# Optimization experiments

Hardware: AMD Instinct MI355X
Metric: run time of the kernel (lower is better)

The kernel has to match this reference:

```python
import jax, jax.numpy as jnp
import numpy as np

R_S, R_T = 16, 8
D_SEG, D_GLB = 64, 128
H_SEG, H_GLB = 2, 4
NL = 2
FF_SEG, FF_GLB = 128, 256
THRESH = 0.5
B, L = 16, 1024


def setup_inputs() -> dict:
    key = jax.random.key(0)
    ks = iter(jax.random.split(key, 40))

    def p(shape, s=0.02):
        return s * jax.random.normal(next(ks), shape, dtype=jnp.float32)

    inp = {}
    inp['pts'] = jax.random.normal(next(ks), (B, L, 3), dtype=jnp.float32)
    # Fourier spatio-temporal encoder params
    inp['fs'] = p((2, R_S), 1.0)                      # spatial frequencies
    inp['ft'] = p((R_T,), 1.0)                        # temporal frequencies
    inp['w_space'] = p((2 * R_S, D_SEG)); inp['b_space'] = p((D_SEG,))
    inp['w_time'] = p((2 * R_T, 32)); inp['b_time'] = p((32,))
    inp['w_fout'] = p((D_SEG + 32, D_SEG)); inp['b_fout'] = p((D_SEG,))
    # gating
    inp['w_gate'] = p((D_SEG,), 1.0); inp['b_gate'] = p(())
    # segment mini-transformer (2 post-norm encoder layers, relu FFN)
    inp['seg_attn_w'] = p((NL, 4, D_SEG, D_SEG)); inp['seg_attn_b'] = p((NL, 4, D_SEG))
    inp['seg_ln_g'] = jnp.ones((NL, 2, D_SEG), jnp.float32)
    inp['seg_ln_b'] = jnp.zeros((NL, 2, D_SEG), jnp.float32)
    inp['seg_ff1_w'] = p((NL, D_SEG, FF_SEG)); inp['seg_ff1_b'] = p((NL, FF_SEG))
    inp['seg_ff2_w'] = p((NL, FF_SEG, D_SEG)); inp['seg_ff2_b'] = p((NL, D_SEG))
    # global aggregator transformer
    inp['glb_attn_w'] = p((NL, 4, D_GLB, D_GLB)); inp['glb_attn_b'] = p((NL, 4, D_GLB))
    inp['glb_ln_g'] = jnp.ones((NL, 2, D_GLB), jnp.float32)
    inp['glb_ln_b'] = jnp.zeros((NL, 2, D_GLB), jnp.float32)
    inp['glb_ff1_w'] = p((NL, D_GLB, FF_GLB)); inp['glb_ff1_b'] = p((NL, FF_GLB))
    inp['glb_ff2_w'] = p((NL, FF_GLB, D_GLB)); inp['glb_ff2_b'] = p((NL, D_GLB))
    # projections
    inp['up_w'] = p((D_SEG, D_GLB)); inp['up_b'] = p((D_GLB,))
    inp['fin_w'] = p((D_GLB, D_GLB)); inp['fin_b'] = p((D_GLB,))
    return inp


def _ln(x, g, b, eps=1e-5):
    m = x.mean(-1, keepdims=True)
    v = ((x - m) ** 2).mean(-1, keepdims=True)
    return (x - m) * jax.lax.rsqrt(v + eps) * g + b


def _mha(x, mask, w, bb, nh):
    Bb, S, D = x.shape
    hd = D // nh
    wq, wk, wv, wo = w
    bq, bk, bv, bo = bb
    q = (x @ wq + bq).reshape(Bb, S, nh, hd)
    k = (x @ wk + bk).reshape(Bb, S, nh, hd)
    v = (x @ wv + bv).reshape(Bb, S, nh, hd)
    sc = jnp.einsum('bqhd,bkhd->bhqk', q, k) / jnp.sqrt(jnp.float32(hd))
    sc = jnp.where(mask[:, None, :, :], sc, jnp.float32(-1e9))
    a = jax.nn.softmax(sc, axis=-1)
    o = jnp.einsum('bhqk,bkhd->bqhd', a, v).reshape(Bb, S, D)
    return o @ wo + bo


def _encoder(x, mask, attn_w, attn_b, ln_g, ln_b, ff1_w, ff1_b, ff2_w, ff2_b, nh):
    # PyTorch-style post-norm TransformerEncoder (dropout=0, eval mode)
    for l in range(attn_w.shape[0]):
        x = _ln(x + _mha(x, mask, attn_w[l], attn_b[l], nh), ln_g[l, 0], ln_b[l, 0])
        h = jax.nn.relu(x @ ff1_w[l] + ff1_b[l]) @ ff2_w[l] + ff2_b[l]
        x = _ln(x + h, ln_g[l, 1], ln_b[l, 1])
    return x


def reference(pts, fs, ft, w_space, b_space, w_time, b_time, w_fout, b_fout, w_gate, b_gate, seg_attn_w, seg_attn_b, seg_ln_g, seg_ln_b, seg_ff1_w, seg_ff1_b, seg_ff2_w, seg_ff2_b, glb_attn_w, glb_attn_b, glb_ln_g, glb_ln_b, glb_ff1_w, glb_ff1_b, glb_ff2_w, glb_ff2_b, up_w, up_b, fin_w, fin_b):
    Bb, Ll, _ = pts.shape
    two_pi = jnp.float32(2.0 * np.pi)
    xy, t = pts[..., :2], pts[..., 2:3]
    # Fourier features (space + time), fused into d=64 point embedding z
    sp = xy @ fs * two_pi                                        # [B,L,r_s]
    sp_feat = jnp.concatenate([jnp.sin(sp), jnp.cos(sp)], -1) @ w_space + b_space
    tp = t * ft * two_pi                                         # [B,L,r_t]
    t_feat = jnp.concatenate([jnp.sin(tp), jnp.cos(tp)], -1) @ w_time + b_time
    z = jnp.concatenate([sp_feat, t_feat], -1) @ w_fout + b_fout  # [B,L,64]

    # dynamic segmentation gating: boundary where sigmoid gate > threshold
    gate = jax.nn.sigmoid(z @ w_gate + b_gate)                   # [B,L]
    boundary = (gate > THRESH).at[:, 0].set(True)
    seg_id = jnp.cumsum(boundary.astype(jnp.int32), axis=1) - 1  # [B,L] contiguous ids
    n_seg = seg_id[:, -1] + 1                                    # [B]

    # segment mini-transformer == full-length transformer with within-segment attention mask
    seg_mask = seg_id[:, :, None] == seg_id[:, None, :]          # [B,L,L]
    h = _encoder(z, seg_mask, seg_attn_w, seg_attn_b, seg_ln_g, seg_ln_b,
                 seg_ff1_w, seg_ff1_b, seg_ff2_w, seg_ff2_b, H_SEG)

    # per-segment mean pooling (padded to L segment slots)
    sums = jax.vmap(lambda hh, sid: jax.ops.segment_sum(hh, sid, num_segments=Ll))(h, seg_id)
    cnts = jax.vmap(lambda sid: jax.ops.segment_sum(jnp.ones((Ll,), jnp.float32), sid, num_segments=Ll))(seg_id)
    seg_emb = sums / jnp.maximum(cnts, 1.0)[..., None]           # [B,L,64]
    valid = jnp.arange(Ll)[None, :] < n_seg[:, None]             # [B,L]
    seg_emb = jnp.where(valid[..., None], seg_emb @ up_w + up_b, 0.0)  # [B,L,128]

    # global aggregator over valid segment embeddings (padding-masked)
    glb_mask = (valid[:, None, :] & valid[:, :, None]) | jnp.eye(Ll, dtype=bool)[None]
    g = _encoder(seg_emb, glb_mask, glb_attn_w, glb_attn_b, glb_ln_g, glb_ln_b,
                 glb_ff1_w, glb_ff1_b, glb_ff2_w, glb_ff2_b, H_GLB)
    agg = (g * valid[..., None]).sum(1) / n_seg[:, None].astype(jnp.float32)

    # single-segment trajectories skip the global aggregator
    global_emb = jnp.where((n_seg == 1)[:, None], seg_emb[:, 0, :], agg)
    return global_emb @ fin_w + fin_b                            # [B,128]
```

## Files before the change

### kernel.cpp

```cpp
#include <hip/hip_runtime.h>
#include <math.h>

#define B_ 16
#define L_ 1024
#define M_TOT (B_*L_)

typedef __attribute__((ext_vector_type(8))) short short8v;
typedef __attribute__((ext_vector_type(4))) float f32x4;

__device__ __forceinline__ float wave_reduce_sum(float v) {
#pragma unroll
  for (int o = 32; o >= 1; o >>= 1) v += __shfl_xor(v, o, 64);
  return v;
}

__device__ __forceinline__ unsigned short f2bf(float f) {
  union { float f; unsigned u; } v; v.f = f;
  unsigned r = v.u + 0x7FFFu + ((v.u >> 16) & 1u);
  return (unsigned short)(r >> 16);
}

__global__ __launch_bounds__(256) void pack_all_kernel(
    const float* __restrict__ s0, const float* __restrict__ s1,
    const float* __restrict__ s2, const float* __restrict__ s3,
    const float* __restrict__ s4, const float* __restrict__ s5,
    const float* __restrict__ s6, unsigned short* __restrict__ wpk)
{
  int idx = blockIdx.x*256 + (int)threadIdx.x;
  const float* src; unsigned short* dst; int K, N;
  if      (idx <  4096) { src=s0; dst=wpk;          K=64;  N=64;  }
  else if (idx <  6144) { src=s1; dst=wpk+32768;    K=64;  N=128; idx-=4096; }
  else if (idx <  8192) { src=s2; dst=wpk+49152;    K=128; N=64;  idx-=6144; }
  else if (idx < 24576) { src=s3; dst=wpk+65536;    K=128; N=128; idx-=8192; }
  else if (idx < 32768) { src=s4; dst=wpk+196608;   K=128; N=256; idx-=24576; }
  else if (idx < 40960) { src=s5; dst=wpk+262144;   K=256; N=128; idx-=32768; }
  else if (idx < 41984) { src=s6; dst=wpk+327680;   K=64;  N=128; idx-=40960; }
  else return;
  const int l = idx & 63;
  int f = idx >> 6;
  const int ntn = N >> 4;
  const int nt = f % ntn; f /= ntn;
  const int ktn = K >> 5;
  const int kt = f % ktn;
  const int m  = f / ktn;
  const float* s = src + (size_t)m*K*N + (size_t)(kt*32 + ((l>>4)<<3))*N + nt*16 + (l&15);
  unsigned pw[4];
#pragma unroll
  for (int jj = 0; jj < 4; ++jj)
    pw[jj] = (unsigned)f2bf(s[(size_t)(2*jj)*N]) | ((unsigned)f2bf(s[(size_t)(2*jj+1)*N]) << 16);
  uint4 u; u.x = pw[0]; u.y = pw[1]; u.z = pw[2]; u.w = pw[3];
  *reinterpret_cast<uint4*>(dst + (size_t)idx*8) = u;
}

template<int K, int PN, int NPARTS, bool RELU, bool GATED, bool WF32, bool WBF, int SPART = -1>
__global__ __launch_bounds__(256) void mgemm_kernel(
    const unsigned short* __restrict__ Abf,
    const unsigned short* __restrict__ Wpk,
    const float* __restrict__ bias,
    float* __restrict__ C, unsigned short* __restrict__ Cbf,
    const int* __restrict__ nseg)
{
  constexpr int NOUT = NPARTS*PN;
  constexpr int KT = K/32;
  constexpr int NTP = PN/16;
  constexpr int CPP = PN/64;
  const int row0 = blockIdx.x * 64;
  if (GATED) { const int b = row0 >> 10; if ((row0 & (L_-1)) >= nseg[b]) return; }
  const int ct = blockIdx.y;
  const int part = ct / CPP;
  const int nt0  = (ct % CPP) * 4;
  const int wv = (int)threadIdx.x >> 6;
  const int ln = (int)threadIdx.x & 63;
  const int rbase = row0 + wv*16;
  const unsigned short* aptr = Abf + (size_t)(rbase + (ln & 15))*K + ((ln >> 4) << 3);
  const unsigned short* bptr = Wpk + ((size_t)part*KT*NTP + nt0)*512 + (size_t)ln*8;
  f32x4 acc0 = {0.f,0.f,0.f,0.f}, acc1 = {0.f,0.f,0.f,0.f};
  f32x4 acc2 = {0.f,0.f,0.f,0.f}, acc3 = {0.f,0.f,0.f,0.f};
#pragma unroll
  for (int kt = 0; kt < KT; ++kt) {
    short8v a = *reinterpret_cast<const short8v*>(aptr + kt*32);
    const unsigned short* bk = bptr + (size_t)kt*NTP*512;
    short8v b0 = *reinterpret_cast<const short8v*>(bk);
    short8v b1 = *reinterpret_cast<const short8v*>(bk + 512);
    short8v b2 = *reinterpret_cast<const short8v*>(bk + 1024);
    short8v b3 = *reinterpret_cast<const short8v*>(bk + 1536);
    acc0 = __builtin_amdgcn_mfma_f32_16x16x32_bf16(a, b0, acc0, 0, 0, 0);
    acc1 = __builtin_amdgcn_mfma_f32_16x16x32_bf16(a, b1, acc1, 0, 0, 0);
    acc2 = __builtin_amdgcn_mfma_f32_16x16x32_bf16(a, b2, acc2, 0, 0, 0);
    acc3 = __builtin_amdgcn_mfma_f32_16x16x32_bf16(a, b3, acc3, 0, 0, 0);
  }
  const int colb = part*PN + nt0*16 + (ln & 15);
  const int rowe = rbase + ((ln >> 4) << 2);
  f32x4 av[4] = {acc0, acc1, acc2, acc3};
#pragma unroll
  for (int i = 0; i < 4; ++i) {
    const int col = colb + i*16;
    const float bs = bias[col];
#pragma unroll
    for (int r = 0; r < 4; ++r) {
      float v = av[i][r] + bs;
      if (SPART >= 0) { if (part == SPART) v *= 0.25506972533f; }
      if (RELU) v = fmaxf(v, 0.f);
      if (WF32) C[(size_t)(rowe + r)*NOUT + col] = v;
      if (WBF)  Cbf[(size_t)(rowe + r)*NOUT + col] = f2bf(v);
    }
  }
}

template<int K>
__global__ __launch_bounds__(256) void mgemm_ln64_kernel(
    const unsigned short* __restrict__ Abf,
    const unsigned short* __restrict__ Wpk,
    const float* __restrict__ bias,
    float* __restrict__ x,
    const float* __restrict__ gam, const float* __restrict__ bet,
    unsigned short* __restrict__ xbf)
{
  constexpr int KT = K/32;
  const int row0 = blockIdx.x * 64;
  const int wv = (int)threadIdx.x >> 6;
  const int ln = (int)threadIdx.x & 63;
  const int rbase = row0 + wv*16;
  const unsigned short* aptr = Abf + (size_t)(rbase + (ln & 15))*K + ((ln >> 4) << 3);
  const unsigned short* bptr = Wpk + (size_t)ln*8;
  f32x4 acc0 = {0.f,0.f,0.f,0.f}, acc1 = {0.f,0.f,0.f,0.f};
  f32x4 acc2 = {0.f,0.f,0.f,0.f}, acc3 = {0.f,0.f,0.f,0.f};
#pragma unroll
  for (int kt = 0; kt < KT; ++kt) {
    short8v a = *reinterpret_cast<const short8v*>(aptr + kt*32);
    const unsigned short* bk = bptr + (size_t)kt*4*512;
    short8v b0 = *reinterpret_cast<const short8v*>(bk);
    short8v b1 = *reinterpret_cast<const short8v*>(bk + 512);
    short8v b2 = *reinterpret_cast<const short8v*>(bk + 1024);
    short8v b3 = *reinterpret_cast<const short8v*>(bk + 1536);
    acc0 = __builtin_amdgcn_mfma_f32_16x16x32_bf16(a, b0, acc0, 0, 0, 0);
    acc1 = __builtin_amdgcn_mfma_f32_16x16x32_bf16(a, b1, acc1, 0, 0, 0);
    acc2 = __builtin_amdgcn_mfma_f32_16x16x32_bf16(a, b2, acc2, 0, 0, 0);
    acc3 = __builtin_amdgcn_mfma_f32_16x16x32_bf16(a, b3, acc3, 0, 0, 0);
  }
  const int colc = ln & 15;
  const int rowe = rbase + ((ln >> 4) << 2);
  f32x4 av[4] = {acc0, acc1, acc2, acc3};
  float v[4][4];
#pragma unroll
  for (int i = 0; i < 4; ++i) {
    const int col = i*16 + colc;
    const float bs = bias[col];
#pragma unroll
    for (int r = 0; r < 4; ++r)
      v[i][r] = av[i][r] + bs + x[(size_t)(rowe + r)*64 + col];
  }
  float rs[4];
#pragma unroll
  for (int r = 0; r < 4; ++r) rs[r] = v[0][r]+v[1][r]+v[2][r]+v[3][r];
#pragma unroll
  for (int m = 1; m <= 8; m <<= 1)
#pragma unroll
    for (int r = 0; r < 4; ++r) rs[r] += __shfl_xor(rs[r], m, 64);
  float mean[4], vs[4];
#pragma unroll
  for (int r = 0; r < 4; ++r) { mean[r] = rs[r]*(1.0f/64.0f); vs[r] = 0.f; }
#pragma unroll
  for (int i = 0; i < 4; ++i)
#pragma unroll
    for (int r = 0; r < 4; ++r) { const float d = v[i][r]-mean[r]; vs[r] = fmaf(d, d, vs[r]); }
#pragma unroll
  for (int m = 1; m <= 8; m <<= 1)
#pragma unroll
    for (int r = 0; r < 4; ++r) vs[r] += __shfl_xor(vs[r], m, 64);
  float rstd[4];
#pragma unroll
  for (int r = 0; r < 4; ++r) rstd[r] = rsqrtf(vs[r]*(1.0f/64.0f) + 1e-5f);
#pragma unroll
  for (int i = 0; i < 4; ++i) {
    const int col = i*16 + colc;
    const float g = gam[col], bb = bet[col];
#pragma unroll
    for (int r = 0; r < 4; ++r) {
      const float out = (v[i][r]-mean[r])*rstd[r]*g + bb;
      x[(size_t)(rowe + r)*64 + col] = out;
      xbf[(size_t)(rowe + r)*64 + col] = f2bf(out);
    }
  }
}

__global__ __launch_bounds__(256) void featurize_kernel(
    const float* __restrict__ pts, const float* __restrict__ fs, const float* __restrict__ ft,
    const float* __restrict__ w_space, const float* __restrict__ b_space,
    const float* __restrict__ w_time, const float* __restrict__ b_time,
    const float* __restrict__ w_fout, const float* __restrict__ b_fout,
    const float* __restrict__ w_gate, const float* __restrict__ b_gate,
    float* __restrict__ z, unsigned short* __restrict__ zbf, int* __restrict__ boundary)
{
  const int sub = threadIdx.x >> 6;
  const int d   = threadIdx.x & 63;
  const int p   = blockIdx.x * 4 + sub;
  const float TWO_PI = 6.283185307179586f;
  __shared__ float feat[4][32];
  __shared__ float tfeat[4][16];
  __shared__ float g96[4][96];
  const float x = pts[p*3+0], y = pts[p*3+1], t = pts[p*3+2];
  if (d < 16) {
    float sp = (x*fs[d] + y*fs[16+d]) * TWO_PI;
    feat[sub][d]    = sinf(sp);
    feat[sub][16+d] = cosf(sp);
  } else if (d < 24) {
    int r = d - 16;
    float tp = t * ft[r] * TWO_PI;
    tfeat[sub][r]   = sinf(tp);
    tfeat[sub][8+r] = cosf(tp);
  }
  __syncthreads();
  float sf = b_space[d];
#pragma unroll
  for (int k2 = 0; k2 < 32; ++k2) sf = fmaf(feat[sub][k2], w_space[k2*64+d], sf);
  g96[sub][d] = sf;
  if (d < 32) {
    float tf = b_time[d];
#pragma unroll
    for (int k2 = 0; k2 < 16; ++k2) tf = fmaf(tfeat[sub][k2], w_time[k2*32+d], tf);
    g96[sub][64+d] = tf;
  }
  __syncthreads();
  float zv = b_fout[d];
#pragma unroll
  for (int k2 = 0; k2 < 96; ++k2) zv = fmaf(g96[sub][k2], w_fout[k2*64+d], zv);
  z[(size_t)p*64+d] = zv;
  zbf[(size_t)p*64+d] = f2bf(zv);
  float gv = wave_reduce_sum(zv * w_gate[d]);
  if (d == 0) {
    float logit = gv + b_gate[0];
    float gate = 1.0f / (1.0f + expf(-logit));
    int bnd = (gate > 0.5f) ? 1 : 0;
    if ((p & (L_-1)) == 0) bnd = 1;
    boundary[p] = bnd;
  }
}

__global__ __launch_bounds__(1024) void scan_kernel(const int* __restrict__ boundary,
    int* __restrict__ seg_id, int* __restrict__ seg_start, int* __restrict__ n_seg)
{
  __shared__ int sc[1024];
  const int b = blockIdx.x, l = threadIdx.x;
  const int v = boundary[b*L_ + l];
  sc[l] = v;
  __syncthreads();
  for (int off = 1; off < 1024; off <<= 1) {
    int add = (l >= off) ? sc[l - off] : 0;
    __syncthreads();
    sc[l] += add;
    __syncthreads();
  }
  const int sid = sc[l] - 1;
  seg_id[b*L_ + l] = sid;
  if (v) seg_start[b*(L_+1) + sid] = l;
  if (l == L_-1) {
    n_seg[b] = sid + 1;
    seg_start[b*(L_+1) + sid + 1] = L_;
  }
}

__global__ __launch_bounds__(256) void seg_attn_kernel(
    const float* __restrict__ qkv,
    const int* __restrict__ seg_id, const int* __restrict__ seg_start,
    unsigned short* __restrict__ aobf)
{
  const int gid = blockIdx.x * 256 + (int)threadIdx.x;
  const int sub = gid & 7;
  const int item = gid >> 3;
  const int h  = item & 1;
  const int pt = (item >> 1) & (L_-1);
  const int b  = item >> 11;
  const float scale = 0.17677669529663687f;
  float4 q4 = *reinterpret_cast<const float4*>(qkv + (size_t)(b*L_+pt)*192 + h*32 + sub*4);
  q4.x*=scale; q4.y*=scale; q4.z*=scale; q4.w*=scale;
  const int s  = seg_id[b*L_ + pt];
  const int j0 = seg_start[b*(L_+1) + s];
  const int j1 = seg_start[b*(L_+1) + s + 1];
  float lsum = 0.f;
  float4 acc = {0.f,0.f,0.f,0.f};
  for (int j = j0; j < j1; ++j) {
    const float* base = qkv + (size_t)(b*L_ + j)*192 + h*32 + sub*4;
    float4 k4 = *reinterpret_cast<const float4*>(base + 64);
    float4 v4 = *reinterpret_cast<const float4*>(base + 128);
    float dot = q4.x*k4.x;
    dot = fmaf(q4.y, k4.y, dot);
    dot = fmaf(q4.z, k4.z, dot);
    dot = fmaf(q4.w, k4.w, dot);
    dot += __shfl_xor(dot, 1, 64);
    dot += __shfl_xor(dot, 2, 64);
    dot += __shfl_xor(dot, 4, 64);
    const float p = __expf(fminf(dot, 30.f));
    lsum += p;
    acc.x = fmaf(p, v4.x, acc.x);
    acc.y = fmaf(p, v4.y, acc.y);
    acc.z = fmaf(p, v4.z, acc.z);
    acc.w = fmaf(p, v4.w, acc.w);
  }
  const float inv = 1.0f / lsum;
  unsigned* op = reinterpret_cast<unsigned*>(aobf + (size_t)(b*L_+pt)*64 + h*32 + sub*4);
  op[0] = (unsigned)f2bf(acc.x*inv) | ((unsigned)f2bf(acc.y*inv) << 16);
  op[1] = (unsigned)f2bf(acc.z*inv) | ((unsigned)f2bf(acc.w*inv) << 16);
}

__global__ __launch_bounds__(256) void kvpack_kernel(
    const unsigned short* __restrict__ qkvbf, const int* __restrict__ n_seg,
    unsigned short* __restrict__ vfrag, unsigned short* __restrict__ kfrag)
{
  int idx = blockIdx.x*256 + (int)threadIdx.x;
  const bool isK = idx >= (1 << 18);
  idx &= (1 << 18) - 1;
  const int lane = idx & 63;
  const int dt = (idx >> 6) & 1;
  const int c  = (idx >> 7) & 31;
  const int h  = (idx >> 12) & 3;
  const int b  = idx >> 14;
  if (c*32 >= n_seg[b]) return;
  if (isK) {
    const int key = c*32 + dt*16 + (lane & 15);
    const uint4 u = *reinterpret_cast<const uint4*>(
        qkvbf + (size_t)(b*L_ + key)*384 + 128 + h*32 + ((lane >> 4) << 3));
    *reinterpret_cast<uint4*>(kfrag + (size_t)idx*8) = u;
    return;
  }
  const int g = lane >> 4;
  const int dcol = lane & 15;
  unsigned short vals[8];
#pragma unroll
  for (int j = 0; j < 8; ++j) {
    const int key = c*32 + g*4 + (j & 3) + ((j >> 2) << 4);
    vals[j] = qkvbf[(size_t)(b*L_ + key)*384 + 256 + h*32 + dt*16 + dcol];
  }
  uint4 u;
  u.x = (unsigned)vals[0] | ((unsigned)vals[1] << 16);
  u.y = (unsigned)vals[2] | ((unsigned)vals[3] << 16);
  u.z = (unsigned)vals[4] | ((unsigned)vals[5] << 16);
  u.w = (unsigned)vals[6] | ((unsigned)vals[7] << 16);
  *reinterpret_cast<uint4*>(vfrag + (size_t)idx*8) = u;
}

__global__ __launch_bounds__(256) void glb_attn_mfma_kernel(
    const unsigned short* __restrict__ qkvbf,
    const unsigned short* __restrict__ kfrag,
    const unsigned short* __restrict__ vfrag,
    const int* __restrict__ n_seg,
    unsigned short* __restrict__ aobf)
{
  const int g64 = blockIdx.x & 63;
  const int qt  = blockIdx.x >> 6;
  const int h  = g64 & 3;
  const int b  = g64 >> 2;
  const int ns = n_seg[b];
  if (qt*64 >= ns) return;
  const int wv = (int)threadIdx.x >> 6;
  const int ln = (int)threadIdx.x & 63;
  const int g  = ln >> 4;
  const int qc = ln & 15;
  __shared__ float lsumS[4][16];

  const int q0 = qt*64 + wv*16;
  const short8v qf = *reinterpret_cast<const short8v*>(
      qkvbf + (size_t)(b*L_ + q0 + qc)*384 + h*32 + g*8);

  f32x4 O0 = {0.f,0.f,0.f,0.f}, O1 = {0.f,0.f,0.f,0.f};
  const f32x4 zz = {0.f,0.f,0.f,0.f};
  float lsum = 0.f;
  const unsigned short* kfb = kfrag + (size_t)((b*4 + h)*32)*1024 + (size_t)ln*8;
  const unsigned short* vfb = vfrag + (size_t)((b*4 + h)*32)*1024 + (size_t)ln*8;

  const int nfull = ns >> 5;
#pragma unroll 2
  for (int c = 0; c < nfull; ++c) {
    short8v kf0 = *reinterpret_cast<const short8v*>(kfb);
    short8v kf1 = *reinterpret_cast<const short8v*>(kfb + 512);
    short8v v0  = *reinterpret_cast<const short8v*>(vfb);
    short8v v1  = *reinterpret_cast<const short8v*>(vfb + 512);
    f32x4 s0 = __builtin_amdgcn_mfma_f32_16x16x32_bf16(kf0, qf, zz, 0, 0, 0);
    f32x4 s1 = __builtin_amdgcn_mfma_f32_16x16x32_bf16(kf1, qf, zz, 0, 0, 0);
    float p[8];
#pragma unroll
    for (int r = 0; r < 4; ++r) {
      const float e0 = exp2f(fminf(s0[r], 43.f));
      const float e1 = exp2f(fminf(s1[r], 43.f));
      p[r] = e0; p[4+r] = e1;
      lsum += e0 + e1;
    }
    short8v pf;
#pragma unroll
    for (int i = 0; i < 8; ++i) pf[i] = (short)f2bf(p[i]);
    O0 = __builtin_amdgcn_mfma_f32_16x16x32_bf16(pf, v0, O0, 0, 0, 0);
    O1 = __builtin_amdgcn_mfma_f32_16x16x32_bf16(pf, v1, O1, 0, 0, 0);
    kfb += 1024; vfb += 1024;
  }
  if (ns & 31) {
    short8v kf0 = *reinterpret_cast<const short8v*>(kfb);
    short8v kf1 = *reinterpret_cast<const short8v*>(kfb + 512);
    short8v v0  = *reinterpret_cast<const short8v*>(vfb);
    short8v v1  = *reinterpret_cast<const short8v*>(vfb + 512);
    f32x4 s0 = __builtin_amdgcn_mfma_f32_16x16x32_bf16(kf0, qf, zz, 0, 0, 0);
    f32x4 s1 = __builtin_amdgcn_mfma_f32_16x16x32_bf16(kf1, qf, zz, 0, 0, 0);
    const int k0 = nfull*32;
    float p[8];
#pragma unroll
    for (int r = 0; r < 4; ++r) {
      const int key0 = k0 + g*4 + r;
      const float e0 = (key0 < ns)      ? exp2f(fminf(s0[r], 43.f)) : 0.f;
      const float e1 = (key0 + 16 < ns) ? exp2f(fminf(s1[r], 43.f)) : 0.f;
      p[r] = e0; p[4+r] = e1;
      lsum += e0 + e1;
    }
    short8v pf;
#pragma unroll
    for (int i = 0; i < 8; ++i) pf[i] = (short)f2bf(p[i]);
    O0 = __builtin_amdgcn_mfma_f32_16x16x32_bf16(pf, v0, O0, 0, 0, 0);
    O1 = __builtin_amdgcn_mfma_f32_16x16x32_bf16(pf, v1, O1, 0, 0, 0);
  }
  lsum += __shfl_xor(lsum, 16, 64);
  lsum += __shfl_xor(lsum, 32, 64);
  if (ln < 16) lsumS[wv][ln] = lsum;
  __syncthreads();
  unsigned short* outp = aobf + (size_t)(b*L_ + q0 + g*4)*128 + h*32 + qc;
#pragma unroll
  for (int r = 0; r < 4; ++r) {
    const float inv = 1.0f / lsumS[wv][g*4 + r];
    outp[(size_t)r*128]      = f2bf(O0[r]*inv);
    outp[(size_t)r*128 + 16] = f2bf(O1[r]*inv);
  }
}

__global__ __launch_bounds__(256) void ln128_kernel(
    float* __restrict__ x, const float* __restrict__ r,
    const float* __restrict__ gam, const float* __restrict__ bet,
    const int* __restrict__ nseg, unsigned short* __restrict__ xbf)
{
  const int row0 = blockIdx.x*2;
  const int b = row0 >> 10;
  if ((row0 & (L_-1)) >= nseg[b]) return;
  const int sub = (int)threadIdx.x >> 7;
  const int d   = (int)threadIdx.x & 127;
  const int row = row0 + sub;
  const bool valid = (row & (L_-1)) < nseg[b];
  __shared__ float red[2][4];
  float val = 0.f;
  if (valid) val = x[(size_t)row*128 + d] + r[(size_t)row*128 + d];
  float s = wave_reduce_sum(val);
  if ((d & 63) == 0) red[sub][d >> 6] = s;
  __syncthreads();
  s = red[sub][0] + red[sub][1];
  const float mean = s * (1.0f/128.0f);
  const float dv = val - mean;
  float s2 = wave_reduce_sum(dv*dv);
  if ((d & 63) == 0) red[sub][2 + (d >> 6)] = s2;
  __syncthreads();
  s2 = red[sub][2] + red[sub][3];
  if (valid) {
    const float out = dv * rsqrtf(s2*(1.0f/128.0f) + 1e-5f) * gam[d] + bet[d];
    x[(size_t)row*128 + d] = out;
    xbf[(size_t)row*128 + d] = f2bf(out);
  }
}

__global__ __launch_bounds__(256) void pool_kernel(
    const float* __restrict__ h, const int* __restrict__ seg_start,
    const int* __restrict__ n_seg, unsigned short* __restrict__ meanbf)
{
  const int gs = blockIdx.x*4 + ((int)threadIdx.x >> 6);
  const int b = gs >> 10, s = gs & (L_-1);
  const int d = (int)threadIdx.x & 63;
  if (s >= n_seg[b]) return;
  const int j0 = seg_start[b*(L_+1)+s], j1 = seg_start[b*(L_+1)+s+1];
  float acc = 0.f;
  for (int j = j0; j < j1; ++j) acc += h[(size_t)(b*L_+j)*64 + d];
  meanbf[(size_t)gs*64 + d] = f2bf(acc / (float)(j1 - j0));
}

__global__ __launch_bounds__(128) void row0_kernel(
    const float* __restrict__ xg, float* __restrict__ semb0)
{
  semb0[blockIdx.x*128 + threadIdx.x] = xg[(size_t)blockIdx.x*L_*128 + threadIdx.x];
}

__global__ __launch_bounds__(128) void pool_final_kernel(
    const float* __restrict__ g, const int* __restrict__ n_seg,
    float* __restrict__ partial)
{
  const int b = blockIdx.x >> 4, c = blockIdx.x & 15;
  const int d = (int)threadIdx.x;
  const int ns = n_seg[b];
  const int i0 = c*64, i1 = min(ns, i0 + 64);
  float acc = 0.f;
  for (int i = i0; i < i1; ++i) acc += g[(size_t)(b*L_+i)*128 + d];
  partial[(size_t)blockIdx.x*128 + d] = acc;
}

__global__ __launch_bounds__(128) void final_kernel(
    const float* __restrict__ partial, const float* __restrict__ semb0,
    const int* __restrict__ n_seg, const float* __restrict__ fin_w,
    const float* __restrict__ fin_b, float* __restrict__ out)
{
  const int b = blockIdx.x, d = threadIdx.x;
  const int ns = n_seg[b];
  __shared__ float pl[128];
  float pooled;
  if (ns == 1) pooled = semb0[b*128 + d];
  else {
    float acc = 0.f;
#pragma unroll
    for (int c = 0; c < 16; ++c) acc += partial[(size_t)(b*16 + c)*128 + d];
    pooled = acc / (float)ns;
  }
  pl[d] = pooled;
  __syncthreads();
  float o = fin_b[d];
#pragma unroll 8
  for (int k2 = 0; k2 < 128; ++k2) o = fmaf(pl[k2], fin_w[k2*128+d], o);
  out[b*128+d] = o;
}

extern "C" void kernel_launch(void* const* d_in, const int* in_sizes, int n_in,
                              void* d_out, int out_size, void* d_ws, size_t ws_size,
                              hipStream_t stream) {
  const float* pts     = (const float*)d_in[0];
  const float* fs      = (const float*)d_in[1];
  const float* ft      = (const float*)d_in[2];
  const float* w_space = (const float*)d_in[3];
  const float* b_space = (const float*)d_in[4];
  const float* w_time  = (const float*)d_in[5];
  const float* b_time  = (const float*)d_in[6];
  const float* w_fout  = (const float*)d_in[7];
  const float* b_fout  = (const float*)d_in[8];
  const float* w_gate  = (const float*)d_in[9];
  const float* b_gate  = (const float*)d_in[10];
  const float* seg_attn_w = (const float*)d_in[11];
  const float* seg_attn_b = (const float*)d_in[12];
  const float* seg_ln_g   = (const float*)d_in[13];
  const float* seg_ln_b   = (const float*)d_in[14];
  const float* seg_ff1_w  = (const float*)d_in[15];
  const float* seg_ff1_b  = (const float*)d_in[16];
  const float* seg_ff2_w  = (const float*)d_in[17];
  const float* seg_ff2_b  = (const float*)d_in[18];
  const float* glb_attn_w = (const float*)d_in[19];
  const float* glb_attn_b = (const float*)d_in[20];
  const float* glb_ln_g   = (const float*)d_in[21];
  const float* glb_ln_b   = (const float*)d_in[22];
  const float* glb_ff1_w  = (const float*)d_in[23];
  const float* glb_ff1_b  = (const float*)d_in[24];
  const float* glb_ff2_w  = (const float*)d_in[25];
  const float* glb_ff2_b  = (const float*)d_in[26];
  const float* up_w    = (const float*)d_in[27];
  const float* up_b    = (const float*)d_in[28];
  const float* fin_w   = (const float*)d_in[29];
  const float* fin_b   = (const float*)d_in[30];

  char* ws = (char*)d_ws;
  float* zx   = (float*)(ws);
  unsigned short* xg_bf = (unsigned short*)(ws);
  float* qkv  = (float*)(ws + ((size_t)4  << 20));
  unsigned short* qkv_bf = (unsigned short*)(ws + ((size_t)4 << 20));
  float* tmp  = qkv;
  float* aob  = (float*)(ws + ((size_t)30 << 20));
  float* xg   = (float*)(ws + ((size_t)38 << 20));
  unsigned short* zx_bf = (unsigned short*)(ws + ((size_t)38 << 20));
  int* boundary  = (int*)(ws + ((size_t)46 << 20));
  int* seg_id    = boundary + M_TOT;
  int* seg_start = seg_id + M_TOT;
  int* n_seg     = seg_start + B_*(L_+1);
  float* semb0     = (float*)(ws + ((size_t)47 << 20));
  float* partial   = (float*)(ws + ((size_t)47 << 20) + 65536);
  unsigned short* tmp_bf = (unsigned short*)(ws + ((size_t)50 << 20));
  unsigned short* vfrag  = (unsigned short*)(ws + ((size_t)58 << 20));
  unsigned short* kfrag  = (unsigned short*)(ws + ((size_t)62 << 20));
  unsigned short* abf    = (unsigned short*)(ws + ((size_t)84 << 20));
  unsigned short* wpk    = (unsigned short*)(ws + ((size_t)88 << 20));

  unsigned short* wpk_segA  = wpk;
  unsigned short* wpk_segF1 = wpk + 32768;
  unsigned short* wpk_segF2 = wpk + 49152;
  unsigned short* wpk_glbA  = wpk + 65536;
  unsigned short* wpk_glbF1 = wpk + 196608;
  unsigned short* wpk_glbF2 = wpk + 262144;
  unsigned short* wpk_up    = wpk + 327680;

  pack_all_kernel<<<164, 256, 0, stream>>>(seg_attn_w, seg_ff1_w, seg_ff2_w,
                                           glb_attn_w, glb_ff1_w, glb_ff2_w, up_w, wpk);

  featurize_kernel<<<M_TOT/4, 256, 0, stream>>>(pts, fs, ft, w_space, b_space, w_time, b_time,
                                                w_fout, b_fout, w_gate, b_gate, zx, zx_bf, boundary);
  scan_kernel<<<B_, 1024, 0, stream>>>(boundary, seg_id, seg_start, n_seg);

  for (int l = 0; l < 2; ++l) {
    const float* ab = seg_attn_b + (size_t)l*4*64;
    mgemm_kernel<64,64,3,false,false,true,false><<<dim3(256,3),256,0,stream>>>(
        zx_bf, wpk_segA + (size_t)l*4*4096, ab, qkv, nullptr, nullptr);
    seg_attn_kernel<<<(M_TOT*2*8)/256, 256, 0, stream>>>(qkv, seg_id, seg_start, abf);
    mgemm_ln64_kernel<64><<<256,256,0,stream>>>(
        abf, wpk_segA + (size_t)(l*4+3)*4096, ab + 192,
        zx, seg_ln_g + l*128, seg_ln_b + l*128, zx_bf);
    mgemm_kernel<64,128,1,true,false,false,true><<<dim3(256,2),256,0,stream>>>(
        zx_bf, wpk_segF1 + (size_t)l*8192, seg_ff1_b + l*128, nullptr, tmp_bf, nullptr);
    mgemm_ln64_kernel<128><<<256,256,0,stream>>>(
        tmp_bf, wpk_segF2 + (size_t)l*8192, seg_ff2_b + l*64,
        zx, seg_ln_g + l*128 + 64, seg_ln_b + l*128 + 64, zx_bf);
  }

  pool_kernel<<<M_TOT/4, 256, 0, stream>>>(zx, seg_start, n_seg, abf);
  mgemm_kernel<64,128,1,false,true,true,true><<<dim3(256,2),256,0,stream>>>(
      abf, wpk_up, up_b, xg, xg_bf, n_seg);
  row0_kernel<<<B_, 128, 0, stream>>>(xg, semb0);

  for (int l = 0; l < 2; ++l) {
    const float* ab = glb_attn_b + (size_t)l*4*128;
    mgemm_kernel<128,128,3,false,true,false,true,0><<<dim3(256,6),256,0,stream>>>(
        xg_bf, wpk_glbA + (size_t)l*4*16384, ab, nullptr, qkv_bf, n_seg);
    kvpack_kernel<<<2048, 256, 0, stream>>>(qkv_bf, n_seg, vfrag, kfrag);
    glb_attn_mfma_kernel<<<B_*4*16, 256, 0, stream>>>(qkv_bf, kfrag, vfrag, n_seg, abf);
    mgemm_kernel<128,128,1,false,true,true,false><<<dim3(256,2),256,0,stream>>>(
        abf, wpk_glbA + (size_t)(l*4+3)*16384, ab + 384, tmp, nullptr, n_seg);
    ln128_kernel<<<M_TOT/2, 256, 0, stream>>>(xg, tmp, glb_ln_g + l*256, glb_ln_b + l*256, n_seg, xg_bf);
    mgemm_kernel<128,256,1,true,true,false,true><<<dim3(256,4),256,0,stream>>>(
        xg_bf, wpk_glbF1 + (size_t)l*32768, glb_ff1_b + l*256, nullptr, tmp_bf, n_seg);
    mgemm_kernel<256,128,1,false,true,true,false><<<dim3(256,2),256,0,stream>>>(
        tmp_bf, wpk_glbF2 + (size_t)l*32768, glb_ff2_b + l*128, aob, nullptr, n_seg);
    ln128_kernel<<<M_TOT/2, 256, 0, stream>>>(xg, aob, glb_ln_g + l*256 + 128, glb_ln_b + l*256 + 128, n_seg, xg_bf);
  }

  pool_final_kernel<<<B_*16, 128, 0, stream>>>(xg, n_seg, partial);
  final_kernel<<<B_, 128, 0, stream>>>(partial, semb0, n_seg, fin_w, fin_b, (float*)d_out);
}
```

Before: 284.5 us.

## Fuse QKV fragment packing, residual LayerNorm, and row0 copy into global GEMMs

The global QKV GEMM now writes Q as bf16 and scatters K and V straight into the MFMA fragment layouts, which removes the separate kvpack kernel and its round trip through a 384-wide qkv buffer. The output-projection and FF2 GEMMs become full-width 128-column kernels that add the residual and apply LayerNorm in registers, replacing the separate ln128 kernels and their fp32 temporaries. The up-projection GEMM also writes the segment-0 embedding, removing the row0 kernel. In exchange, the K/V scatter uses scattered 2-byte stores, and the fused LN GEMMs launch fewer blocks that each do more work.

```diff
diff --git a/kernel.cpp b/kernel.cpp
--- a/kernel.cpp
+++ b/kernel.cpp
@@ -52,13 +52,14 @@
   *reinterpret_cast<uint4*>(dst + (size_t)idx*8) = u;
 }
 
-template<int K, int PN, int NPARTS, bool RELU, bool GATED, bool WF32, bool WBF, int SPART = -1>
+template<int K, int PN, int NPARTS, bool RELU, bool GATED, bool WF32, bool WBF,
+         int SPART = -1, bool SEMB0 = false>
 __global__ __launch_bounds__(256) void mgemm_kernel(
     const unsigned short* __restrict__ Abf,
     const unsigned short* __restrict__ Wpk,
     const float* __restrict__ bias,
     float* __restrict__ C, unsigned short* __restrict__ Cbf,
-    const int* __restrict__ nseg)
+    const int* __restrict__ nseg, float* __restrict__ semb0)
 {
   constexpr int NOUT = NPARTS*PN;
   constexpr int KT = K/32;
@@ -101,8 +102,72 @@
       float v = av[i][r] + bs;
       if (SPART >= 0) { if (part == SPART) v *= 0.25506972533f; }
       if (RELU) v = fmaxf(v, 0.f);
-      if (WF32) C[(size_t)(rowe + r)*NOUT + col] = v;
-      if (WBF)  Cbf[(size_t)(rowe + r)*NOUT + col] = f2bf(v);
+      const int row = rowe + r;
+      if (WF32) C[(size_t)row*NOUT + col] = v;
+      if (WBF)  Cbf[(size_t)row*NOUT + col] = f2bf(v);
+      if (SEMB0) { if ((row & (L_-1)) == 0) semb0[(row >> 10)*NOUT + col] = v; }
+    }
+  }
+}
+
+__global__ __launch_bounds__(256) void mgemm_qkvfrag_kernel(
+    const unsigned short* __restrict__ Abf,
+    const unsigned short* __restrict__ Wpk,
+    const float* __restrict__ bias,
+    unsigned short* __restrict__ qbf,
+    unsigned short* __restrict__ kfrag,
+    unsigned short* __restrict__ vfrag,
+    const int* __restrict__ nseg)
+{
+  constexpr int K = 128, PN = 128, KT = 4, NTP = 8;
+  const int row0 = blockIdx.x * 64;
+  const int bb = row0 >> 10;
+  if ((row0 & (L_-1)) >= nseg[bb]) return;
+  const int ct = blockIdx.y;
+  const int part = ct >> 1;
+  const int nt0 = (ct & 1) * 4;
+  const int wv = (int)threadIdx.x >> 6;
+  const int ln = (int)threadIdx.x & 63;
+  const int qc = ln & 15;
+  const int rbase = row0 + wv*16;
+  const unsigned short* aptr = Abf + (size_t)(rbase + qc)*K + ((ln >> 4) << 3);
+  const unsigned short* bptr = Wpk + ((size_t)part*KT*NTP + nt0)*512 + (size_t)ln*8;
+  f32x4 acc[4];
+#pragma unroll
+  for (int i = 0; i < 4; ++i) acc[i] = f32x4{0.f,0.f,0.f,0.f};
+#pragma unroll
+  for (int kt = 0; kt < KT; ++kt) {
+    short8v a = *reinterpret_cast<const short8v*>(aptr + kt*32);
+    const unsigned short* bk = bptr + (size_t)kt*NTP*512;
+#pragma unroll
+    for (int i = 0; i < 4; ++i)
+      acc[i] = __builtin_amdgcn_mfma_f32_16x16x32_bf16(
+          a, *reinterpret_cast<const short8v*>(bk + i*512), acc[i], 0, 0, 0);
+  }
+  const int rowe = rbase + ((ln >> 4) << 2);
+#pragma unroll
+  for (int i = 0; i < 4; ++i) {
+    const int cl = (nt0 + i)*16 + qc;
+    const int h = cl >> 5, dh = cl & 31;
+    const float bs = bias[part*PN + cl];
+#pragma unroll
+    for (int r = 0; r < 4; ++r) {
+      float v = acc[i][r] + bs;
+      const int row = rowe + r;
+      const int key = row & (L_-1);
+      if (part == 0) {
+        v *= 0.25506972533f;
+        qbf[(size_t)row*128 + cl] = f2bf(v);
+      } else if (part == 1) {
+        const size_t idx = (((size_t)((bb*4 + h)*32 + (key>>5))*2 + ((key>>4)&1))*64
+                            + ((dh>>3)*16 + (key&15)))*8 + (dh&7);
+        kfrag[idx] = f2bf(v);
+      } else {
+        const int kk = key & 31;
+        const size_t idx = (((size_t)((bb*4 + h)*32 + (key>>5))*2 + (dh>>4))*64
+                            + (((kk&15)>>2)*16 + (dh&15)))*8 + ((kk>>4)*4 + (kk&3));
+        vfrag[idx] = f2bf(v);
+      }
     }
   }
 }
@@ -180,6 +245,81 @@
       const float out = (v[i][r]-mean[r])*rstd[r]*g + bb;
       x[(size_t)(rowe + r)*64 + col] = out;
       xbf[(size_t)(rowe + r)*64 + col] = f2bf(out);
+    }
+  }
+}
+
+template<int K>
+__global__ __launch_bounds__(256) void mgemm_ln128_kernel(
+    const unsigned short* __restrict__ Abf,
+    const unsigned short* __restrict__ Wpk,
+    const float* __restrict__ bias,
+    float* __restrict__ x,
+    const float* __restrict__ gam, const float* __restrict__ bet,
+    const int* __restrict__ nseg, unsigned short* __restrict__ xbf)
+{
+  constexpr int KT = K/32;
+  const int row0 = blockIdx.x * 64;
+  if ((row0 & (L_-1)) >= nseg[row0 >> 10]) return;
+  const int wv = (int)threadIdx.x >> 6;
+  const int ln = (int)threadIdx.x & 63;
+  const int qc = ln & 15;
+  const int rbase = row0 + wv*16;
+  const unsigned short* aptr = Abf + (size_t)(rbase + qc)*K + ((ln >> 4) << 3);
+  const unsigned short* bptr = Wpk + (size_t)ln*8;
+  f32x4 acc[8];
+#pragma unroll
+  for (int i = 0; i < 8; ++i) acc[i] = f32x4{0.f,0.f,0.f,0.f};
+#pragma unroll
+  for (int kt = 0; kt < KT; ++kt) {
+    short8v a = *reinterpret_cast<const short8v*>(aptr + kt*32);
+    const unsigned short* bk = bptr + (size_t)kt*8*512;
+#pragma unroll
+    for (int i = 0; i < 8; ++i)
+      acc[i] = __builtin_amdgcn_mfma_f32_16x16x32_bf16(
+          a, *reinterpret_cast<const short8v*>(bk + i*512), acc[i], 0, 0, 0);
+  }
+  const int rowe = rbase + ((ln >> 4) << 2);
+  float v[8][4];
+#pragma unroll
+  for (int i = 0; i < 8; ++i) {
+    const int col = i*16 + qc;
+    const float bs = bias[col];
+#pragma unroll
+    for (int r = 0; r < 4; ++r)
+      v[i][r] = acc[i][r] + bs + x[(size_t)(rowe + r)*128 + col];
+  }
+  float rs[4];
+#pragma unroll
+  for (int r = 0; r < 4; ++r)
+    rs[r] = ((v[0][r]+v[1][r])+(v[2][r]+v[3][r])) + ((v[4][r]+v[5][r])+(v[6][r]+v[7][r]));
+#pragma unroll
+  for (int m = 1; m <= 8; m <<= 1)
+#pragma unroll
+    for (int r = 0; r < 4; ++r) rs[r] += __shfl_xor(rs[r], m, 64);
+  float mean[4], vs[4];
+#pragma unroll
+  for (int r = 0; r < 4; ++r) { mean[r] = rs[r]*(1.0f/128.0f); vs[r] = 0.f; }
+#pragma unroll
+  for (int i = 0; i < 8; ++i)
+#pragma unroll
+    for (int r = 0; r < 4; ++r) { const float d = v[i][r]-mean[r]; vs[r] = fmaf(d, d, vs[r]); }
+#pragma unroll
+  for (int m = 1; m <= 8; m <<= 1)
+#pragma unroll
+    for (int r = 0; r < 4; ++r) vs[r] += __shfl_xor(vs[r], m, 64);
+  float rstd[4];
+#pragma unroll
+  for (int r = 0; r < 4; ++r) rstd[r] = rsqrtf(vs[r]*(1.0f/128.0f) + 1e-5f);
+#pragma unroll
+  for (int i = 0; i < 8; ++i) {
+    const int col = i*16 + qc;
+    const float g = gam[col], bb = bet[col];
+#pragma unroll
+    for (int r = 0; r < 4; ++r) {
+      const float out = (v[i][r]-mean[r])*rstd[r]*g + bb;
+      x[(size_t)(rowe + r)*128 + col] = out;
+      xbf[(size_t)(rowe + r)*128 + col] = f2bf(out);
     }
   }
 }
@@ -303,44 +443,8 @@
   op[1] = (unsigned)f2bf(acc.z*inv) | ((unsigned)f2bf(acc.w*inv) << 16);
 }
 
-__global__ __launch_bounds__(256) void kvpack_kernel(
-    const unsigned short* __restrict__ qkvbf, const int* __restrict__ n_seg,
-    unsigned short* __restrict__ vfrag, unsigned short* __restrict__ kfrag)
-{
-  int idx = blockIdx.x*256 + (int)threadIdx.x;
-  const bool isK = idx >= (1 << 18);
-  idx &= (1 << 18) - 1;
-  const int lane = idx & 63;
-  const int dt = (idx >> 6) & 1;
-  const int c  = (idx >> 7) & 31;
-  const int h  = (idx >> 12) & 3;
-  const int b  = idx >> 14;
-  if (c*32 >= n_seg[b]) return;
-  if (isK) {
-    const int key = c*32 + dt*16 + (lane & 15);
-    const uint4 u = *reinterpret_cast<const uint4*>(
-        qkvbf + (size_t)(b*L_ + key)*384 + 128 + h*32 + ((lane >> 4) << 3));
-    *reinterpret_cast<uint4*>(kfrag + (size_t)idx*8) = u;
-    return;
-  }
-  const int g = lane >> 4;
-  const int dcol = lane & 15;
-  unsigned short vals[8];
-#pragma unroll
-  for (int j = 0; j < 8; ++j) {
-    const int key = c*32 + g*4 + (j & 3) + ((j >> 2) << 4);
-    vals[j] = qkvbf[(size_t)(b*L_ + key)*384 + 256 + h*32 + dt*16 + dcol];
-  }
-  uint4 u;
-  u.x = (unsigned)vals[0] | ((unsigned)vals[1] << 16);
-  u.y = (unsigned)vals[2] | ((unsigned)vals[3] << 16);
-  u.z = (unsigned)vals[4] | ((unsigned)vals[5] << 16);
-  u.w = (unsigned)vals[6] | ((unsigned)vals[7] << 16);
-  *reinterpret_cast<uint4*>(vfrag + (size_t)idx*8) = u;
-}
-
 __global__ __launch_bounds__(256) void glb_attn_mfma_kernel(
-    const unsigned short* __restrict__ qkvbf,
+    const unsigned short* __restrict__ qbf,
     const unsigned short* __restrict__ kfrag,
     const unsigned short* __restrict__ vfrag,
     const int* __restrict__ n_seg,
@@ -360,7 +464,7 @@
 
   const int q0 = qt*64 + wv*16;
   const short8v qf = *reinterpret_cast<const short8v*>(
-      qkvbf + (size_t)(b*L_ + q0 + qc)*384 + h*32 + g*8);
+      qbf + (size_t)(b*L_ + q0 + qc)*128 + h*32 + g*8);
 
   f32x4 O0 = {0.f,0.f,0.f,0.f}, O1 = {0.f,0.f,0.f,0.f};
   const f32x4 zz = {0.f,0.f,0.f,0.f};
@@ -428,38 +532,6 @@
   }
 }
 
-__global__ __launch_bounds__(256) void ln128_kernel(
-    float* __restrict__ x, const float* __restrict__ r,
-    const float* __restrict__ gam, const float* __restrict__ bet,
-    const int* __restrict__ nseg, unsigned short* __restrict__ xbf)
-{
-  const int row0 = blockIdx.x*2;
-  const int b = row0 >> 10;
-  if ((row0 & (L_-1)) >= nseg[b]) return;
-  const int sub = (int)threadIdx.x >> 7;
-  const int d   = (int)threadIdx.x & 127;
-  const int row = row0 + sub;
-  const bool valid = (row & (L_-1)) < nseg[b];
-  __shared__ float red[2][4];
-  float val = 0.f;
-  if (valid) val = x[(size_t)row*128 + d] + r[(size_t)row*128 + d];
-  float s = wave_reduce_sum(val);
-  if ((d & 63) == 0) red[sub][d >> 6] = s;
-  __syncthreads();
-  s = red[sub][0] + red[sub][1];
-  const float mean = s * (1.0f/128.0f);
-  const float dv = val - mean;
-  float s2 = wave_reduce_sum(dv*dv);
-  if ((d & 63) == 0) red[sub][2 + (d >> 6)] = s2;
-  __syncthreads();
-  s2 = red[sub][2] + red[sub][3];
-  if (valid) {
-    const float out = dv * rsqrtf(s2*(1.0f/128.0f) + 1e-5f) * gam[d] + bet[d];
-    x[(size_t)row*128 + d] = out;
-    xbf[(size_t)row*128 + d] = f2bf(out);
-  }
-}
-
 __global__ __launch_bounds__(256) void pool_kernel(
     const float* __restrict__ h, const int* __restrict__ seg_start,
     const int* __restrict__ n_seg, unsigned short* __restrict__ meanbf)
@@ -472,12 +544,6 @@
   float acc = 0.f;
   for (int j = j0; j < j1; ++j) acc += h[(size_t)(b*L_+j)*64 + d];
   meanbf[(size_t)gs*64 + d] = f2bf(acc / (float)(j1 - j0));
-}
-
-__global__ __launch_bounds__(128) void row0_kernel(
-    const float* __restrict__ xg, float* __restrict__ semb0)
-{
-  semb0[blockIdx.x*128 + threadIdx.x] = xg[(size_t)blockIdx.x*L_*128 + threadIdx.x];
 }
 
 __global__ __launch_bounds__(128) void pool_final_kernel(
@@ -556,9 +622,6 @@
   float* zx   = (float*)(ws);
   unsigned short* xg_bf = (unsigned short*)(ws);
   float* qkv  = (float*)(ws + ((size_t)4  << 20));
-  unsigned short* qkv_bf = (unsigned short*)(ws + ((size_t)4 << 20));
-  float* tmp  = qkv;
-  float* aob  = (float*)(ws + ((size_t)30 << 20));
   float* xg   = (float*)(ws + ((size_t)38 << 20));
   unsigned short* zx_bf = (unsigned short*)(ws + ((size_t)38 << 20));
   int* boundary  = (int*)(ws + ((size_t)46 << 20));
@@ -570,6 +633,7 @@
   unsigned short* tmp_bf = (unsigned short*)(ws + ((size_t)50 << 20));
   unsigned short* vfrag  = (unsigned short*)(ws + ((size_t)58 << 20));
   unsigned short* kfrag  = (unsigned short*)(ws + ((size_t)62 << 20));
+  unsigned short* qbf    = (unsigned short*)(ws + ((size_t)66 << 20));
   unsigned short* abf    = (unsigned short*)(ws + ((size_t)84 << 20));
   unsigned short* wpk    = (unsigned short*)(ws + ((size_t)88 << 20));
 
@@ -591,37 +655,35 @@
   for (int l = 0; l < 2; ++l) {
     const float* ab = seg_attn_b + (size_t)l*4*64;
     mgemm_kernel<64,64,3,false,false,true,false><<<dim3(256,3),256,0,stream>>>(
-        zx_bf, wpk_segA + (size_t)l*4*4096, ab, qkv, nullptr, nullptr);
+        zx_bf, wpk_segA + (size_t)l*4*4096, ab, qkv, nullptr, nullptr, nullptr);
     seg_attn_kernel<<<(M_TOT*2*8)/256, 256, 0, stream>>>(qkv, seg_id, seg_start, abf);
     mgemm_ln64_kernel<64><<<256,256,0,stream>>>(
         abf, wpk_segA + (size_t)(l*4+3)*4096, ab + 192,
         zx, seg_ln_g + l*128, seg_ln_b + l*128, zx_bf);
     mgemm_kernel<64,128,1,true,false,false,true><<<dim3(256,2),256,0,stream>>>(
-        zx_bf, wpk_segF1 + (size_t)l*8192, seg_ff1_b + l*128, nullptr, tmp_bf, nullptr);
+        zx_bf, wpk_segF1 + (size_t)l*8192, seg_ff1_b + l*128, nullptr, tmp_bf, nullptr, nullptr);
     mgemm_ln64_kernel<128><<<256,256,0,stream>>>(
         tmp_bf, wpk_segF2 + (size_t)l*8192, seg_ff2_b + l*64,
         zx, seg_ln_g + l*128 + 64, seg_ln_b + l*128 + 64, zx_bf);
   }
 
   pool_kernel<<<M_TOT/4, 256, 0, stream>>>(zx, seg_start, n_seg, abf);
-  mgemm_kernel<64,128,1,false,true,true,true><<<dim3(256,2),256,0,stream>>>(
-      abf, wpk_up, up_b, xg, xg_bf, n_seg);
-  row0_kernel<<<B_, 128, 0, stream>>>(xg, semb0);
+  mgemm_kernel<64,128,1,false,true,true,true,-1,true><<<dim3(256,2),256,0,stream>>>(
+      abf, wpk_up, up_b, xg, xg_bf, n_seg, semb0);
 
   for (int l = 0; l < 2; ++l) {
     const float* ab = glb_attn_b + (size_t)l*4*128;
-    mgemm_kernel<128,128,3,false,true,false,true,0><<<dim3(256,6),256,0,stream>>>(
-        xg_bf, wpk_glbA + (size_t)l*4*16384, ab, nullptr, qkv_bf, n_seg);
-    kvpack_kernel<<<2048, 256, 0, stream>>>(qkv_bf, n_seg, vfrag, kfrag);
-    glb_attn_mfma_kernel<<<B_*4*16, 256, 0, stream>>>(qkv_bf, kfrag, vfrag, n_seg, abf);
-    mgemm_kernel<128,128,1,false,true,true,false><<<dim3(256,2),256,0,stream>>>(
-        abf, wpk_glbA + (size_t)(l*4+3)*16384, ab + 384, tmp, nullptr, n_seg);
-    ln128_kernel<<<M_TOT/2, 256, 0, stream>>>(xg, tmp, glb_ln_g + l*256, glb_ln_b + l*256, n_seg, xg_bf);
+    mgemm_qkvfrag_kernel<<<dim3(256,6),256,0,stream>>>(
+        xg_bf, wpk_glbA + (size_t)l*4*16384, ab, qbf, kfrag, vfrag, n_seg);
+    glb_attn_mfma_kernel<<<B_*4*16, 256, 0, stream>>>(qbf, kfrag, vfrag, n_seg, abf);
+    mgemm_ln128_kernel<128><<<256,256,0,stream>>>(
+        abf, wpk_glbA + (size_t)(l*4+3)*16384, ab + 384,
+        xg, glb_ln_g + l*256, glb_ln_b + l*256, n_seg, xg_bf);
     mgemm_kernel<128,256,1,true,true,false,true><<<dim3(256,4),256,0,stream>>>(
-        xg_bf, wpk_glbF1 + (size_t)l*32768, glb_ff1_b + l*256, nullptr, tmp_bf, n_seg);
-    mgemm_kernel<256,128,1,false,true,true,false><<<dim3(256,2),256,0,stream>>>(
-        tmp_bf, wpk_glbF2 + (size_t)l*32768, glb_ff2_b + l*128, aob, nullptr, n_seg);
-    ln128_kernel<<<M_TOT/2, 256, 0, stream>>>(xg, aob, glb_ln_g + l*256 + 128, glb_ln_b + l*256 + 128, n_seg, xg_bf);
+        xg_bf, wpk_glbF1 + (size_t)l*32768, glb_ff1_b + l*256, nullptr, tmp_bf, n_seg, nullptr);
+    mgemm_ln128_kernel<256><<<256,256,0,stream>>>(
+        tmp_bf, wpk_glbF2 + (size_t)l*32768, glb_ff2_b + l*128,
+        xg, glb_ln_g + l*256 + 128, glb_ln_b + l*256 + 128, n_seg, xg_bf);
   }
 
   pool_final_kernel<<<B_*16, 128, 0, stream>>>(xg, n_seg, partial);
```

Measured after the change: 237.2 us. 16.6% less time.
